# Kernel optimization log

Measured on AMD Instinct MI355X. Metric: run time of the kernel, lower is better.

## Reference

```python
import jax, jax.numpy as jnp
import numpy as np
import math

HIDDEN = 1024
NUM_HEADS = 16
HEAD_DIM = HIDDEN // NUM_HEADS
B, S = 4, 1024


def setup_inputs() -> dict:
    key = jax.random.key(0)
    ks = jax.random.split(key, 16)
    sd = 1.0 / math.sqrt(HIDDEN)
    inp = {
        "x": jax.random.normal(ks[0], (B, S, HIDDEN), jnp.float32),
        "spikes": jax.random.uniform(ks[1], (B, S, HIDDEN), jnp.float32),
        "membrane_potential": jax.random.normal(ks[2], (B, S, HIDDEN), jnp.float32),
        "Wq": jax.random.normal(ks[3], (HIDDEN, HIDDEN), jnp.float32) * sd,
        "bq": jnp.zeros((HIDDEN,), jnp.float32),
        "Wk": jax.random.normal(ks[4], (HIDDEN, HIDDEN), jnp.float32) * sd,
        "bk": jnp.zeros((HIDDEN,), jnp.float32),
        "Wv": jax.random.normal(ks[5], (HIDDEN, HIDDEN), jnp.float32) * sd,
        "bv": jnp.zeros((HIDDEN,), jnp.float32),
        "Wo": jax.random.normal(ks[6], (HIDDEN, HIDDEN), jnp.float32) * sd,
        "bo": jnp.zeros((HIDDEN,), jnp.float32),
        "tau_decay": jnp.ones((NUM_HEADS,), jnp.float32) * 10.0,
        "Wg": jax.random.normal(ks[7], (HIDDEN, 2 * HIDDEN), jnp.float32) * sd,
        "bg": jnp.zeros((HIDDEN,), jnp.float32),
    }
    return inp


def _heads(t):  # [B,S,H] -> [B,nH,S,hd]
    Bv, Sv, _ = t.shape
    return t.reshape(Bv, Sv, NUM_HEADS, HEAD_DIM).transpose(0, 2, 1, 3)


def reference(x, spikes, membrane_potential, Wq, bq, Wk, bk, Wv, bv, Wo, bo, tau_decay, Wg, bg):
    scale = 1.0 / math.sqrt(HEAD_DIM)
    q = _heads(x @ Wq.T + bq)
    k = _heads(x @ Wk.T + bk)
    v = _heads(x @ Wv.T + bv)

    # raw scores [B,nH,S,S]
    scores = jnp.einsum('bhqd,bhkd->bhqk', q, k) * scale

    # per-head exponential temporal decay mask [nH,S,S]
    times = jnp.arange(S, dtype=jnp.float32)
    tdiff = jnp.abs(times[:, None] - times[None, :])  # [S,S]
    tmask = jnp.exp(-tdiff[None] / tau_decay[:, None, None])
    scores = scores * tmask[None]

    # spike correlation term
    sm = _heads(spikes)
    spike_attn = jnp.einsum('bhqd,bhkd->bhqk', sm, sm) * scale
    scores = scores * (1.0 + spike_attn)

    # membrane gating of V
    v = v * jax.nn.sigmoid(_heads(membrane_potential))

    probs = jax.nn.softmax(scores, axis=-1)
    context = jnp.einsum('bhqk,bhkd->bhqd', probs, v)
    context = context.transpose(0, 2, 1, 3).reshape(B, S, HIDDEN)

    # dendritic gate
    gate_in = jnp.concatenate([context, membrane_potential], axis=-1)
    gate = jax.nn.sigmoid(gate_in @ Wg.T + bg)
    context = context * gate

    return context @ Wo.T + bo
```

## Files before the change

### kernel.cpp

```cpp
#include <hip/hip_runtime.h>
#include <math.h>
#include <stdint.h>

namespace {

typedef __attribute__((ext_vector_type(8))) short s8v;
typedef __attribute__((ext_vector_type(4))) float f4v;
typedef unsigned short u16;

__device__ __forceinline__ float fexp2(float x) {
  return __builtin_amdgcn_exp2f(x);
}

__device__ __forceinline__ u16 f2bf(float f) {
  union { float f; uint32_t u; } v; v.f = f;
  uint32_t r = v.u + 0x7fffu + ((v.u >> 16) & 1u);
  return (u16)(r >> 16);
}
__device__ __forceinline__ float bf2f(u16 h) {
  union { uint32_t u; float f; } v; v.u = ((uint32_t)h) << 16;
  return v.f;
}
__device__ __forceinline__ uint32_t pk2r(float a, float b) {
  return (uint32_t)f2bf(a) | ((uint32_t)f2bf(b) << 16);
}
__device__ __forceinline__ uint32_t pk2(float a, float b) {
  union { float f; uint32_t u; } x, y; x.f = a; y.f = b;
  return ((x.u + 0x8000u) >> 16) | ((y.u + 0x8000u) & 0xffff0000u);
}
__device__ __forceinline__ float sigmoidf_(float x) { return 1.0f / (1.0f + __expf(-x)); }

__device__ __forceinline__ void gload16(const u16* g, u16* l) {
  __builtin_amdgcn_global_load_lds(
      (const __attribute__((address_space(1))) void*)g,
      (__attribute__((address_space(3))) void*)l, 16, 0, 0);
}

struct CvtJob { const float* src; u16* dst; };
struct CvtArgs { CvtJob j[14]; };

__global__ __launch_bounds__(256) void cvt_kernel(CvtArgs a) {
  const CvtJob jb = a.j[blockIdx.y];
  const int i = blockIdx.x * 256 + threadIdx.x;
  const float4 v = ((const float4*)jb.src)[i];
  uint2 pk;
  pk.x = pk2r(v.x, v.y);
  pk.y = pk2r(v.z, v.w);
  ((uint2*)jb.dst)[i] = pk;
}

__global__ __launch_bounds__(256) void qkv_gemm(
    const u16* __restrict__ xb,
    const u16* __restrict__ Wqb, const u16* __restrict__ Wkb, const u16* __restrict__ Wvb,
    const float* __restrict__ bq, const float* __restrict__ bk, const float* __restrict__ bv,
    const float* __restrict__ mem,
    u16* __restrict__ Qb, u16* __restrict__ Kb, u16* __restrict__ Vt) {
  __shared__ u16 as_[8192], bs_[8192];
  const int t = threadIdx.x;
  const int nb = blockIdx.x, mb = blockIdx.y;
  const int sel = nb >> 3;
  const u16* W = sel == 0 ? Wqb : (sel == 1 ? Wkb : Wvb);
  const float* bias = sel == 0 ? bq : (sel == 1 ? bk : bv);
  const int m0 = mb * 128, n0 = (nb & 7) * 128;
  const f4v fz = {0.f, 0.f, 0.f, 0.f};
  f4v acc[4][4];
#pragma unroll
  for (int i = 0; i < 4; ++i)
#pragma unroll
    for (int j = 0; j < 4; ++j) acc[i][j] = fz;

  const int l = t & 63, w = t >> 6, wm = w >> 1, wn = w & 1;
  const int lr = l & 15, lq = l >> 4;
  const int rx = lr & 7;
  const int srow = t >> 3;
  const int scol = ((t & 7) ^ (srow & 7)) * 8;

#define QKV_STAGE(k0)                                                          \
  {                                                                            \
    const int kk_ = (k0);                                                      \
    _Pragma("unroll") for (int u = 0; u < 4; ++u) {                            \
      gload16(xb + (size_t)(m0 + u * 32 + srow) * 1024 + kk_ + scol,           \
              as_ + u * 2048 + t * 8);                                         \
      gload16(W + (size_t)(n0 + u * 32 + srow) * 1024 + kk_ + scol,            \
              bs_ + u * 2048 + t * 8);                                         \
    }                                                                          \
  }

  QKV_STAGE(0);

  if (sel < 2) {
    for (int c = 0; c < 16; ++c) {
      __syncthreads();
      s8v af[2][4], bf[2][4];
#pragma unroll
      for (int ks = 0; ks < 2; ++ks) {
        const int co = ((ks * 4 + lq) ^ rx) * 8;
#pragma unroll
        for (int mi = 0; mi < 4; ++mi)
          af[ks][mi] = *(const s8v*)(as_ + (wm * 64 + mi * 16 + lr) * 64 + co);
#pragma unroll
        for (int ni = 0; ni < 4; ++ni)
          bf[ks][ni] = *(const s8v*)(bs_ + (wn * 64 + ni * 16 + lr) * 64 + co);
      }
      __syncthreads();
      if (c < 15) QKV_STAGE((c + 1) << 6);
#pragma unroll
      for (int ks = 0; ks < 2; ++ks)
#pragma unroll
        for (int mi = 0; mi < 4; ++mi)
#pragma unroll
          for (int ni = 0; ni < 4; ++ni)
            acc[mi][ni] = __builtin_amdgcn_mfma_f32_16x16x32_bf16(
                bf[ks][ni], af[ks][mi], acc[mi][ni], 0, 0, 0);
    }
    u16* dst = (sel == 0) ? Qb : Kb;
#pragma unroll
    for (int mi = 0; mi < 4; ++mi)
#pragma unroll
      for (int ni = 0; ni < 4; ++ni) {
        const int m = m0 + wm * 64 + mi * 16 + lr;
        const int nb4 = n0 + wn * 64 + ni * 16 + lq * 4;
        const float4 b4 = *(const float4*)&bias[nb4];
        uint2 pk;
        pk.x = pk2r(acc[mi][ni][0] + b4.x, acc[mi][ni][1] + b4.y);
        pk.y = pk2r(acc[mi][ni][2] + b4.z, acc[mi][ni][3] + b4.w);
        *(uint2*)(dst + (size_t)m * 1024 + nb4) = pk;
      }
  } else {
    for (int c = 0; c < 16; ++c) {
      __syncthreads();
      s8v af[2][4], bf[2][4];
#pragma unroll
      for (int ks = 0; ks < 2; ++ks) {
        const int co = ((ks * 4 + lq) ^ rx) * 8;
#pragma unroll
        for (int mi = 0; mi < 4; ++mi)
          af[ks][mi] = *(const s8v*)(as_ + (wm * 64 + mi * 16 + lr) * 64 + co);
#pragma unroll
        for (int ni = 0; ni < 4; ++ni)
          bf[ks][ni] = *(const s8v*)(bs_ + (wn * 64 + ni * 16 + lr) * 64 + co);
      }
      __syncthreads();
      if (c < 15) QKV_STAGE((c + 1) << 6);
#pragma unroll
      for (int ks = 0; ks < 2; ++ks)
#pragma unroll
        for (int mi = 0; mi < 4; ++mi)
#pragma unroll
          for (int ni = 0; ni < 4; ++ni)
            acc[mi][ni] = __builtin_amdgcn_mfma_f32_16x16x32_bf16(
                af[ks][mi], bf[ks][ni], acc[mi][ni], 0, 0, 0);
    }
    const int b = m0 >> 10;
#pragma unroll
    for (int mi = 0; mi < 4; ++mi)
#pragma unroll
      for (int ni = 0; ni < 4; ++ni) {
        const int mrow = m0 + wm * 64 + mi * 16 + lq * 4;
        const int ncol = n0 + wn * 64 + ni * 16 + lr;
        const int h = ncol >> 6, d = ncol & 63;
        const float bi = bias[ncol];
        float tv[4];
#pragma unroll
        for (int r = 0; r < 4; ++r)
          tv[r] = (acc[mi][ni][r] + bi) * sigmoidf_(mem[(size_t)(mrow + r) * 1024 + ncol]);
        const int s = mrow & 1023;
        uint2 pk;
        pk.x = pk2r(tv[0], tv[1]);
        pk.y = pk2r(tv[2], tv[3]);
        *(uint2*)(Vt + ((size_t)((b * 16 + h) * 64 + d)) * 1024 + s) = pk;
      }
  }
#undef QKV_STAGE
}

template <int MODE>
__global__ __launch_bounds__(256) void gemm64(
    const u16* __restrict__ Ab, const u16* __restrict__ A2b,
    const u16* __restrict__ W, const float* __restrict__ bias,
    u16* __restrict__ outb, float* __restrict__ outf, int K) {
  __shared__ u16 as_[4096], bs_[8192];
  const int t = threadIdx.x, l = t & 63, w = t >> 6;
  const int wm = w >> 1, wn = w & 1, lr = l & 15, lq = l >> 4;
  const int m0 = blockIdx.y * 64, n0 = blockIdx.x * 128;
  const f4v fz = {0.f, 0.f, 0.f, 0.f};
  f4v acc[2][4];
#pragma unroll
  for (int i = 0; i < 2; ++i)
#pragma unroll
    for (int j = 0; j < 4; ++j) acc[i][j] = fz;
  const int rx = lr & 7;
  const int srow = t >> 3;
  const int scol = ((t & 7) ^ (srow & 7)) * 8;
  const int nc = K >> 6;

#define G64_STAGE(k0)                                                          \
  {                                                                            \
    const int kk_ = (k0);                                                      \
    const u16* Ae_ = Ab;                                                       \
    int ka_ = kk_;                                                             \
    if (MODE == 1 && kk_ >= 1024) { Ae_ = A2b; ka_ = kk_ - 1024; }             \
    _Pragma("unroll") for (int u = 0; u < 2; ++u)                              \
        gload16(Ae_ + (size_t)(m0 + u * 32 + srow) * 1024 + ka_ + scol,        \
                as_ + u * 2048 + t * 8);                                       \
    _Pragma("unroll") for (int u = 0; u < 4; ++u)                              \
        gload16(W + (size_t)(n0 + u * 32 + srow) * K + kk_ + scol,             \
                bs_ + u * 2048 + t * 8);                                       \
  }

  G64_STAGE(0);
  for (int c = 0; c < nc; ++c) {
    __syncthreads();
    s8v af[2][2], bf[2][4];
#pragma unroll
    for (int ks = 0; ks < 2; ++ks) {
      const int co = ((ks * 4 + lq) ^ rx) * 8;
#pragma unroll
      for (int mi = 0; mi < 2; ++mi)
        af[ks][mi] = *(const s8v*)(as_ + (wm * 32 + mi * 16 + lr) * 64 + co);
#pragma unroll
      for (int ni = 0; ni < 4; ++ni)
        bf[ks][ni] = *(const s8v*)(bs_ + (wn * 64 + ni * 16 + lr) * 64 + co);
    }
    __syncthreads();
    if (c + 1 < nc) G64_STAGE((c + 1) << 6);
#pragma unroll
    for (int ks = 0; ks < 2; ++ks)
#pragma unroll
      for (int mi = 0; mi < 2; ++mi)
#pragma unroll
        for (int ni = 0; ni < 4; ++ni)
          acc[mi][ni] = __builtin_amdgcn_mfma_f32_16x16x32_bf16(
              bf[ks][ni], af[ks][mi], acc[mi][ni], 0, 0, 0);
  }
#undef G64_STAGE

#pragma unroll
  for (int mi = 0; mi < 2; ++mi)
#pragma unroll
    for (int ni = 0; ni < 4; ++ni) {
      const int m = m0 + wm * 32 + mi * 16 + lr;
      const int nb4 = n0 + wn * 64 + ni * 16 + lq * 4;
      const float4 b4 = *(const float4*)&bias[nb4];
      if (MODE == 0) {
        float4 o;
        o.x = acc[mi][ni][0] + b4.x; o.y = acc[mi][ni][1] + b4.y;
        o.z = acc[mi][ni][2] + b4.z; o.w = acc[mi][ni][3] + b4.w;
        *(float4*)(outf + (size_t)m * 1024 + nb4) = o;
      } else {
        const uint2 a2 = *(const uint2*)(Ab + (size_t)m * 1024 + nb4);
        float cx[4] = {bf2f((u16)(a2.x & 0xffff)), bf2f((u16)(a2.x >> 16)),
                       bf2f((u16)(a2.y & 0xffff)), bf2f((u16)(a2.y >> 16))};
        float g[4];
        g[0] = cx[0] * sigmoidf_(acc[mi][ni][0] + b4.x);
        g[1] = cx[1] * sigmoidf_(acc[mi][ni][1] + b4.y);
        g[2] = cx[2] * sigmoidf_(acc[mi][ni][2] + b4.z);
        g[3] = cx[3] * sigmoidf_(acc[mi][ni][3] + b4.w);
        uint2 pk;
        pk.x = pk2r(g[0], g[1]);
        pk.y = pk2r(g[2], g[3]);
        *(uint2*)(outb + (size_t)m * 1024 + nb4) = pk;
      }
    }
}

__global__ __launch_bounds__(256) void attn_mfma(
    const u16* __restrict__ Qb, const u16* __restrict__ Kb,
    const u16* __restrict__ SPb, const u16* __restrict__ Vt,
    const float* __restrict__ tau, u16* __restrict__ CTXb) {
  __shared__ u16 kbuf[4096], skbuf[4096], vbuf[4096];
  __shared__ u16 pbuf[4][16 * 64];
  const int t = threadIdx.x, l = t & 63, w = t >> 6;
  const int lr = l & 15, lq = l >> 4;
  const int p = blockIdx.x;
  const int g = (p & 7) + 8 * (p >> 7);
  const int qt = (p >> 3) & 15;
  const int h = g & 15, b = g >> 4;

  const float c2 = 1.44269504088896f / tau[h];
  const float K0 = 0.125f * 1.44269504088896f;
  float cN[4], cNi[4], cR[4], cRi[4];
#pragma unroll
  for (int i = 0; i < 4; ++i) {
    cN[i]  = fexp2(c2 * (float)(i * 16));
    cNi[i] = fexp2(-c2 * (float)(i * 16));
    cR[i]  = fexp2(c2 * (float)(lq * 4 + i));
    cRi[i] = fexp2(-c2 * (float)(lq * 4 + i));
  }

  s8v qf[2], sf[2];
  {
    const size_t base = ((size_t)(b * 1024 + qt * 64 + w * 16 + lr)) * 1024 + h * 64 + lq * 8;
    qf[0] = *(const s8v*)(Qb + base);
    qf[1] = *(const s8v*)(Qb + base + 32);
    sf[0] = *(const s8v*)(SPb + base);
    sf[1] = *(const s8v*)(SPb + base + 32);
  }

  const f4v fz = {0.f, 0.f, 0.f, 0.f};
  f4v oacc[4];
  float lacc[4];
#pragma unroll
  for (int i = 0; i < 4; ++i) { oacc[i] = fz; lacc[i] = 0.f; }

  const int iqw = qt * 64 + w * 16;
  const int srow = t >> 3;
  const int csw = ((t & 7) ^ (srow & 7)) * 8;
  const int rx = lr & 7;
  u16* pw = pbuf[w];

  for (int jc = 0; jc < 16; ++jc) {
    const int j0 = jc * 64;
    __syncthreads();
    {
      const size_t kg = ((size_t)(b * 1024 + j0 + srow)) * 1024 + h * 64 + csw;
      gload16(Kb + kg, kbuf + t * 8);
      gload16(Kb + kg + 32 * 1024, kbuf + 2048 + t * 8);
      gload16(SPb + kg, skbuf + t * 8);
      gload16(SPb + kg + 32 * 1024, skbuf + 2048 + t * 8);
      const size_t vg = ((size_t)((b * 16 + h) * 64 + srow)) * 1024 + j0 + csw;
      gload16(Vt + vg, vbuf + t * 8);
      gload16(Vt + vg + 32 * 1024, vbuf + 2048 + t * 8);
    }
    __syncthreads();

    f4v sa[4], ssa[4];
#pragma unroll
    for (int ni = 0; ni < 4; ++ni) { sa[ni] = fz; ssa[ni] = fz; }
#pragma unroll
    for (int ks = 0; ks < 2; ++ks) {
#pragma unroll
      for (int ni = 0; ni < 4; ++ni) {
        const int off = (ni * 16 + lr) * 64 + (((ks * 4 + lq) ^ rx) * 8);
        const s8v kf = *(const s8v*)(kbuf + off);
        sa[ni] = __builtin_amdgcn_mfma_f32_16x16x32_bf16(kf, qf[ks], sa[ni], 0, 0, 0);
        const s8v skf = *(const s8v*)(skbuf + off);
        ssa[ni] = __builtin_amdgcn_mfma_f32_16x16x32_bf16(skf, sf[ks], ssa[ni], 0, 0, 0);
      }
    }

    const int D0 = iqw - j0;
    float pv[4][4];
    if (jc < qt) {
      const float EA = K0 * fexp2(-c2 * (float)(D0 + lr));
#pragma unroll
      for (int ni = 0; ni < 4; ++ni)
#pragma unroll
        for (int r = 0; r < 4; ++r) {
          const float t1 = fmaf(ssa[ni][r], 0.125f, 1.0f);
          const float sc2 = sa[ni][r] * cN[ni] * cR[r] * EA * t1;
          const float e = fexp2(sc2);
          pv[ni][r] = e;
          lacc[ni] += e;
        }
    } else if (jc > qt) {
      const float EAi = K0 * fexp2(c2 * (float)(D0 + lr));
#pragma unroll
      for (int ni = 0; ni < 4; ++ni)
#pragma unroll
        for (int r = 0; r < 4; ++r) {
          const float t1 = fmaf(ssa[ni][r], 0.125f, 1.0f);
          const float sc2 = sa[ni][r] * cNi[ni] * cRi[r] * EAi * t1;
          const float e = fexp2(sc2);
          pv[ni][r] = e;
          lacc[ni] += e;
        }
    } else {
      const float EA  = K0 * fexp2(-c2 * (float)(D0 + lr));
      const float EAi = K0 * fexp2(c2 * (float)(D0 + lr));
#pragma unroll
      for (int ni = 0; ni < 4; ++ni)
#pragma unroll
        for (int r = 0; r < 4; ++r) {
          const int jloc = ni * 16 + lq * 4 + r;
          const float fb = cN[ni] * cR[r] * EA;
          const float fa = cNi[ni] * cRi[r] * EAi;
          const float f = (D0 + lr >= jloc) ? fb : fa;
          const float t1 = fmaf(ssa[ni][r], 0.125f, 1.0f);
          const float e = fexp2(sa[ni][r] * f * t1);
          pv[ni][r] = e;
          lacc[ni] += e;
        }
    }

#pragma unroll
    for (int ni = 0; ni < 4; ++ni) {
      const int phys = (ni * 2 + (lq >> 1)) ^ rx;
      uint2 p2;
      p2.x = pk2(pv[ni][0], pv[ni][1]);
      p2.y = pk2(pv[ni][2], pv[ni][3]);
      *(uint2*)(pw + lr * 64 + phys * 8 + (lq & 1) * 4) = p2;
    }

#pragma unroll
    for (int ks = 0; ks < 2; ++ks) {
      const s8v pf = *(const s8v*)(pw + lr * 64 + (((ks * 4 + lq) ^ rx) * 8));
#pragma unroll
      for (int nd = 0; nd < 4; ++nd) {
        const int off = (nd * 16 + lr) * 64 + (((ks * 4 + lq) ^ rx) * 8);
        const s8v vf = *(const s8v*)(vbuf + off);
        oacc[nd] = __builtin_amdgcn_mfma_f32_16x16x32_bf16(vf, pf, oacc[nd], 0, 0, 0);
      }
    }
  }

  float ls = (lacc[0] + lacc[1]) + (lacc[2] + lacc[3]);
  ls += __shfl_xor(ls, 16);
  ls += __shfl_xor(ls, 32);
  const float inv = 1.0f / ls;
  const size_t orow = ((size_t)(b * 1024 + qt * 64 + w * 16 + lr)) * 1024 + h * 64;
#pragma unroll
  for (int nd = 0; nd < 4; ++nd) {
    uint2 o;
    o.x = pk2r(oacc[nd][0] * inv, oacc[nd][1] * inv);
    o.y = pk2r(oacc[nd][2] * inv, oacc[nd][3] * inv);
    *(uint2*)(CTXb + orow + nd * 16 + lq * 4) = o;
  }
}

}

extern "C" void kernel_launch(void* const* d_in, const int* in_sizes, int n_in,
                              void* d_out, int out_size, void* d_ws, size_t ws_size,
                              hipStream_t stream) {
  const float* x      = (const float*)d_in[0];
  const float* spikes = (const float*)d_in[1];
  const float* mem    = (const float*)d_in[2];
  const float* Wq     = (const float*)d_in[3];
  const float* bq     = (const float*)d_in[4];
  const float* Wk     = (const float*)d_in[5];
  const float* bk     = (const float*)d_in[6];
  const float* Wv     = (const float*)d_in[7];
  const float* bv     = (const float*)d_in[8];
  const float* Wo     = (const float*)d_in[9];
  const float* bo     = (const float*)d_in[10];
  const float* tau    = (const float*)d_in[11];
  const float* Wg     = (const float*)d_in[12];
  const float* bg     = (const float*)d_in[13];
  float* out = (float*)d_out;

  uint8_t* w8 = (uint8_t*)d_ws;
  u16* spb  = (u16*)(w8);
  u16* xb   = (u16*)(w8 + (8u << 20));
  u16* Wqb  = (u16*)(w8 + (16u << 20));
  u16* Wkb  = (u16*)(w8 + (18u << 20));
  u16* Wvb  = (u16*)(w8 + (20u << 20));
  u16* Wob  = (u16*)(w8 + (22u << 20));
  u16* Wgb  = (u16*)(w8 + (24u << 20));
  u16* Qb   = (u16*)(w8 + (28u << 20));
  u16* Kb   = (u16*)(w8 + (36u << 20));
  u16* Vt   = (u16*)(w8 + (44u << 20));
  u16* CTXb = (u16*)(w8 + (52u << 20));
  u16* memb = Qb;
  u16* gctx = xb;

  constexpr size_t QE = 262144 * 4;
  CvtArgs ca;
  for (int q = 0; q < 4; ++q) ca.j[q]     = {x + q * QE,      xb + q * QE};
  for (int q = 0; q < 4; ++q) ca.j[4 + q] = {spikes + q * QE, spb + q * QE};
  ca.j[8]  = {Wq, Wqb};
  ca.j[9]  = {Wk, Wkb};
  ca.j[10] = {Wv, Wvb};
  ca.j[11] = {Wo, Wob};
  ca.j[12] = {Wg, Wgb};
  ca.j[13] = {Wg + QE, Wgb + QE};
  cvt_kernel<<<dim3(1024, 14), 256, 0, stream>>>(ca);

  qkv_gemm<<<dim3(24, 32), 256, 0, stream>>>(xb, Wqb, Wkb, Wvb, bq, bk, bv, mem,
                                             Qb, Kb, Vt);
  attn_mfma<<<dim3(1024), 256, 0, stream>>>(Qb, Kb, spb, Vt, tau, CTXb);

  CvtArgs cm;
  for (int q = 0; q < 4; ++q) cm.j[q] = {mem + q * QE, memb + q * QE};
  cvt_kernel<<<dim3(1024, 4), 256, 0, stream>>>(cm);

  gemm64<1><<<dim3(8, 64), 256, 0, stream>>>(CTXb, memb, Wgb, bg, gctx, nullptr, 2048);
  gemm64<0><<<dim3(8, 64), 256, 0, stream>>>(gctx, nullptr, Wob, bo, nullptr, out, 1024);
}
```

Measured before the change: 278.1 us.

## Double-buffer attention K/V loads, MFMA row sums, fold mem conversion into cvt

```diff
diff --git a/kernel.cpp b/kernel.cpp
--- a/kernel.cpp
+++ b/kernel.cpp
@@ -24,9 +24,9 @@
 __device__ __forceinline__ uint32_t pk2r(float a, float b) {
   return (uint32_t)f2bf(a) | ((uint32_t)f2bf(b) << 16);
 }
-__device__ __forceinline__ uint32_t pk2(float a, float b) {
+__device__ __forceinline__ uint32_t pk2p(float a, float b) {
   union { float f; uint32_t u; } x, y; x.f = a; y.f = b;
-  return ((x.u + 0x8000u) >> 16) | ((y.u + 0x8000u) & 0xffff0000u);
+  return __builtin_amdgcn_perm(y.u + 0x8000u, x.u + 0x8000u, 0x07060302u);
 }
 __device__ __forceinline__ float sigmoidf_(float x) { return 1.0f / (1.0f + __expf(-x)); }
 
@@ -37,7 +37,7 @@
 }
 
 struct CvtJob { const float* src; u16* dst; };
-struct CvtArgs { CvtJob j[14]; };
+struct CvtArgs { CvtJob j[18]; };
 
 __global__ __launch_bounds__(256) void cvt_kernel(CvtArgs a) {
   const CvtJob jb = a.j[blockIdx.y];
@@ -268,25 +268,26 @@
     const u16* __restrict__ Qb, const u16* __restrict__ Kb,
     const u16* __restrict__ SPb, const u16* __restrict__ Vt,
     const float* __restrict__ tau, u16* __restrict__ CTXb) {
-  __shared__ u16 kbuf[4096], skbuf[4096], vbuf[4096];
-  __shared__ u16 pbuf[4][16 * 64];
+  __shared__ u16 kbuf[8192], skbuf[8192], vbuf[8192];
+  __shared__ u16 pbuf[4][1024];
   const int t = threadIdx.x, l = t & 63, w = t >> 6;
   const int lr = l & 15, lq = l >> 4;
-  const int p = blockIdx.x;
-  const int g = (p & 7) + 8 * (p >> 7);
-  const int qt = (p >> 3) & 15;
+  const int pid = blockIdx.x;
+  const int g = (pid & 7) + 8 * (pid >> 7);
+  const int qt = (pid >> 3) & 15;
   const int h = g & 15, b = g >> 4;
 
   const float c2 = 1.44269504088896f / tau[h];
   const float K0 = 0.125f * 1.44269504088896f;
-  float cN[4], cNi[4], cR[4], cRi[4];
-#pragma unroll
-  for (int i = 0; i < 4; ++i) {
-    cN[i]  = fexp2(c2 * (float)(i * 16));
-    cNi[i] = fexp2(-c2 * (float)(i * 16));
-    cR[i]  = fexp2(c2 * (float)(lq * 4 + i));
-    cRi[i] = fexp2(-c2 * (float)(lq * 4 + i));
-  }
+  float cNR[4][4], cNRi[4][4];
+#pragma unroll
+  for (int ni = 0; ni < 4; ++ni)
+#pragma unroll
+    for (int r = 0; r < 4; ++r) {
+      const float d = c2 * (float)(ni * 16 + lq * 4 + r);
+      cNR[ni][r]  = fexp2(d);
+      cNRi[ni][r] = fexp2(-d);
+    }
 
   s8v qf[2], sf[2];
   {
@@ -296,12 +297,12 @@
     sf[0] = *(const s8v*)(SPb + base);
     sf[1] = *(const s8v*)(SPb + base + 32);
   }
+  const s8v ones = {0x3F80, 0x3F80, 0x3F80, 0x3F80, 0x3F80, 0x3F80, 0x3F80, 0x3F80};
 
   const f4v fz = {0.f, 0.f, 0.f, 0.f};
-  f4v oacc[4];
-  float lacc[4];
-#pragma unroll
-  for (int i = 0; i < 4; ++i) { oacc[i] = fz; lacc[i] = 0.f; }
+  f4v oacc[4], osum = fz;
+#pragma unroll
+  for (int i = 0; i < 4; ++i) oacc[i] = fz;
 
   const int iqw = qt * 64 + w * 16;
   const int srow = t >> 3;
@@ -309,20 +310,26 @@
   const int rx = lr & 7;
   u16* pw = pbuf[w];
 
+  auto stage = [&](int jc2, int pp) {
+    const int j0s = jc2 * 64;
+    const int lo = pp * 4096;
+    const size_t kg = ((size_t)(b * 1024 + j0s + srow)) * 1024 + h * 64 + csw;
+    gload16(Kb + kg, kbuf + lo + t * 8);
+    gload16(Kb + kg + 32 * 1024, kbuf + lo + 2048 + t * 8);
+    gload16(SPb + kg, skbuf + lo + t * 8);
+    gload16(SPb + kg + 32 * 1024, skbuf + lo + 2048 + t * 8);
+    const size_t vg = ((size_t)((b * 16 + h) * 64 + srow)) * 1024 + j0s + csw;
+    gload16(Vt + vg, vbuf + lo + t * 8);
+    gload16(Vt + vg + 32 * 1024, vbuf + lo + 2048 + t * 8);
+  };
+
+  stage(0, 0);
+  int pp = 0;
   for (int jc = 0; jc < 16; ++jc) {
     const int j0 = jc * 64;
     __syncthreads();
-    {
-      const size_t kg = ((size_t)(b * 1024 + j0 + srow)) * 1024 + h * 64 + csw;
-      gload16(Kb + kg, kbuf + t * 8);
-      gload16(Kb + kg + 32 * 1024, kbuf + 2048 + t * 8);
-      gload16(SPb + kg, skbuf + t * 8);
-      gload16(SPb + kg + 32 * 1024, skbuf + 2048 + t * 8);
-      const size_t vg = ((size_t)((b * 16 + h) * 64 + srow)) * 1024 + j0 + csw;
-      gload16(Vt + vg, vbuf + t * 8);
-      gload16(Vt + vg + 32 * 1024, vbuf + 2048 + t * 8);
-    }
-    __syncthreads();
+    if (jc < 15) stage(jc + 1, pp ^ 1);
+    const int lo = pp * 4096;
 
     f4v sa[4], ssa[4];
 #pragma unroll
@@ -331,7 +338,7 @@
     for (int ks = 0; ks < 2; ++ks) {
 #pragma unroll
       for (int ni = 0; ni < 4; ++ni) {
-        const int off = (ni * 16 + lr) * 64 + (((ks * 4 + lq) ^ rx) * 8);
+        const int off = lo + (ni * 16 + lr) * 64 + (((ks * 4 + lq) ^ rx) * 8);
         const s8v kf = *(const s8v*)(kbuf + off);
         sa[ni] = __builtin_amdgcn_mfma_f32_16x16x32_bf16(kf, qf[ks], sa[ni], 0, 0, 0);
         const s8v skf = *(const s8v*)(skbuf + off);
@@ -348,10 +355,7 @@
 #pragma unroll
         for (int r = 0; r < 4; ++r) {
           const float t1 = fmaf(ssa[ni][r], 0.125f, 1.0f);
-          const float sc2 = sa[ni][r] * cN[ni] * cR[r] * EA * t1;
-          const float e = fexp2(sc2);
-          pv[ni][r] = e;
-          lacc[ni] += e;
+          pv[ni][r] = fexp2(sa[ni][r] * (cNR[ni][r] * EA) * t1);
         }
     } else if (jc > qt) {
       const float EAi = K0 * fexp2(c2 * (float)(D0 + lr));
@@ -360,10 +364,7 @@
 #pragma unroll
         for (int r = 0; r < 4; ++r) {
           const float t1 = fmaf(ssa[ni][r], 0.125f, 1.0f);
-          const float sc2 = sa[ni][r] * cNi[ni] * cRi[r] * EAi * t1;
-          const float e = fexp2(sc2);
-          pv[ni][r] = e;
-          lacc[ni] += e;
+          pv[ni][r] = fexp2(sa[ni][r] * (cNRi[ni][r] * EAi) * t1);
         }
     } else {
       const float EA  = K0 * fexp2(-c2 * (float)(D0 + lr));
@@ -373,13 +374,9 @@
 #pragma unroll
         for (int r = 0; r < 4; ++r) {
           const int jloc = ni * 16 + lq * 4 + r;
-          const float fb = cN[ni] * cR[r] * EA;
-          const float fa = cNi[ni] * cRi[r] * EAi;
-          const float f = (D0 + lr >= jloc) ? fb : fa;
+          const float f = (D0 + lr >= jloc) ? cNR[ni][r] * EA : cNRi[ni][r] * EAi;
           const float t1 = fmaf(ssa[ni][r], 0.125f, 1.0f);
-          const float e = fexp2(sa[ni][r] * f * t1);
-          pv[ni][r] = e;
-          lacc[ni] += e;
+          pv[ni][r] = fexp2(sa[ni][r] * f * t1);
         }
     }
 
@@ -387,27 +384,26 @@
     for (int ni = 0; ni < 4; ++ni) {
       const int phys = (ni * 2 + (lq >> 1)) ^ rx;
       uint2 p2;
-      p2.x = pk2(pv[ni][0], pv[ni][1]);
-      p2.y = pk2(pv[ni][2], pv[ni][3]);
+      p2.x = pk2p(pv[ni][0], pv[ni][1]);
+      p2.y = pk2p(pv[ni][2], pv[ni][3]);
       *(uint2*)(pw + lr * 64 + phys * 8 + (lq & 1) * 4) = p2;
     }
 
 #pragma unroll
     for (int ks = 0; ks < 2; ++ks) {
       const s8v pf = *(const s8v*)(pw + lr * 64 + (((ks * 4 + lq) ^ rx) * 8));
+      osum = __builtin_amdgcn_mfma_f32_16x16x32_bf16(ones, pf, osum, 0, 0, 0);
 #pragma unroll
       for (int nd = 0; nd < 4; ++nd) {
-        const int off = (nd * 16 + lr) * 64 + (((ks * 4 + lq) ^ rx) * 8);
+        const int off = lo + (nd * 16 + lr) * 64 + (((ks * 4 + lq) ^ rx) * 8);
         const s8v vf = *(const s8v*)(vbuf + off);
         oacc[nd] = __builtin_amdgcn_mfma_f32_16x16x32_bf16(vf, pf, oacc[nd], 0, 0, 0);
       }
     }
-  }
-
-  float ls = (lacc[0] + lacc[1]) + (lacc[2] + lacc[3]);
-  ls += __shfl_xor(ls, 16);
-  ls += __shfl_xor(ls, 32);
-  const float inv = 1.0f / ls;
+    pp ^= 1;
+  }
+
+  const float inv = 1.0f / osum[0];
   const size_t orow = ((size_t)(b * 1024 + qt * 64 + w * 16 + lr)) * 1024 + h * 64;
 #pragma unroll
   for (int nd = 0; nd < 4; ++nd) {
@@ -451,29 +447,25 @@
   u16* Kb   = (u16*)(w8 + (36u << 20));
   u16* Vt   = (u16*)(w8 + (44u << 20));
   u16* CTXb = (u16*)(w8 + (52u << 20));
-  u16* memb = Qb;
+  u16* memb = (u16*)d_out;
   u16* gctx = xb;
 
   constexpr size_t QE = 262144 * 4;
   CvtArgs ca;
   for (int q = 0; q < 4; ++q) ca.j[q]     = {x + q * QE,      xb + q * QE};
   for (int q = 0; q < 4; ++q) ca.j[4 + q] = {spikes + q * QE, spb + q * QE};
-  ca.j[8]  = {Wq, Wqb};
-  ca.j[9]  = {Wk, Wkb};
-  ca.j[10] = {Wv, Wvb};
-  ca.j[11] = {Wo, Wob};
-  ca.j[12] = {Wg, Wgb};
-  ca.j[13] = {Wg + QE, Wgb + QE};
-  cvt_kernel<<<dim3(1024, 14), 256, 0, stream>>>(ca);
+  for (int q = 0; q < 4; ++q) ca.j[8 + q] = {mem + q * QE,    memb + q * QE};
+  ca.j[12] = {Wq, Wqb};
+  ca.j[13] = {Wk, Wkb};
+  ca.j[14] = {Wv, Wvb};
+  ca.j[15] = {Wo, Wob};
+  ca.j[16] = {Wg, Wgb};
+  ca.j[17] = {Wg + QE, Wgb + QE};
+  cvt_kernel<<<dim3(1024, 18), 256, 0, stream>>>(ca);
 
   qkv_gemm<<<dim3(24, 32), 256, 0, stream>>>(xb, Wqb, Wkb, Wvb, bq, bk, bv, mem,
                                              Qb, Kb, Vt);
   attn_mfma<<<dim3(1024), 256, 0, stream>>>(Qb, Kb, spb, Vt, tau, CTXb);
-
-  CvtArgs cm;
-  for (int q = 0; q < 4; ++q) cm.j[q] = {mem + q * QE, memb + q * QE};
-  cvt_kernel<<<dim3(1024, 4), 256, 0, stream>>>(cm);
-
   gemm64<1><<<dim3(8, 64), 256, 0, stream>>>(CTXb, memb, Wgb, bg, gctx, nullptr, 2048);
   gemm64<0><<<dim3(8, 64), 256, 0, stream>>>(gctx, nullptr, Wob, bo, nullptr, out, 1024);
 }
```

New measurement: 272.6 us. -2.0%, faster.
